# Kernel tuning notes

Hardware: AMD Instinct MI355X
Metric: run time of the kernel (lower is better)

Reference implementation:

```python
import jax, jax.numpy as jnp
import numpy as np

B = 128                      # num_graphs (cell lines per batch)
SIZES = [706, 512, 256, 128] # nodes per graph at each level; final_node = 128
DIM = 256                    # dim_cell
DEG = 8                      # avg degree of gene-gene network
EPS = 1e-5                   # BatchNorm eps


def _build_graph():
    """Build per-graph edges (incl. self-loops, as GATConv adds) and predefined
    cluster assignments per layer, coarsening edges exactly like PyG max_pool
    (remove self-loops + coalesce). Replicated across B graphs with offsets."""
    rng = np.random.default_rng(0)
    e = rng.integers(0, SIZES[0], size=(2, SIZES[0] * DEG))
    e = e[:, e[0] != e[1]]
    e = np.unique(e, axis=1)
    edges, clusters = [], []
    cur = e
    for i in range(3):
        n_cur, n_next = SIZES[i], SIZES[i + 1]
        sl = np.arange(n_cur)
        e_sl = np.concatenate([cur, np.stack([sl, sl])], axis=1)  # add self-loops
        off = np.arange(B) * n_cur
        eg = (e_sl[:, None, :] + off[None, :, None]).reshape(2, -1)
        edges.append(eg.astype(np.int32))
        cl = np.concatenate([np.arange(n_next), rng.integers(0, n_next, size=n_cur - n_next)])
        rng.shuffle(cl)  # surjective cluster assignment n_cur -> n_next
        clg = (cl[None, :] + (np.arange(B) * n_next)[:, None]).reshape(-1)
        clusters.append(clg.astype(np.int32))
        src, dst = cl[cur[0]], cl[cur[1]]
        m = src != dst                      # pool_edge: remove self-loops
        cur = np.unique(np.stack([src[m], dst[m]]), axis=1)  # coalesce
    return edges, clusters


def setup_inputs() -> dict:
    edges, clusters = _build_graph()
    key = jax.random.key(0)
    ks = jax.random.split(key, 16)
    d = {"x": jax.random.normal(ks[0], (B * SIZES[0], 3), jnp.float32)}
    ins = [3, DIM, DIM]
    for i in range(3):
        s = 1.0 / np.sqrt(ins[i])
        a = 1.0 / np.sqrt(DIM)
        d[f"W{i}"] = jax.random.normal(ks[1 + i], (ins[i], DIM), jnp.float32) * s
        d[f"asrc{i}"] = jax.random.normal(ks[4 + i], (DIM,), jnp.float32) * a
        d[f"adst{i}"] = jax.random.normal(ks[7 + i], (DIM,), jnp.float32) * a
        d[f"b{i}"] = jnp.zeros((DIM,), jnp.float32)
        d[f"edge{i}"] = jnp.asarray(edges[i])
        d[f"cluster{i}"] = jnp.asarray(clusters[i])
    return d


def _gat(x, edge, W, a_s, a_d, b):
    """PyG GATConv, heads=1, negative_slope=0.2 (self-loops pre-added in edge)."""
    N = x.shape[0]
    h = x @ W                                    # [N, D]
    src, dst = edge[0], edge[1]
    e = jax.nn.leaky_relu((h * a_s).sum(-1)[src] + (h * a_d).sum(-1)[dst], 0.2)
    m = jax.ops.segment_max(e, dst, num_segments=N)     # segment softmax (stable)
    ex = jnp.exp(e - m[dst])
    ssum = jax.ops.segment_sum(ex, dst, num_segments=N)
    alpha = ex / ssum[dst]
    out = jax.ops.segment_sum(h[src] * alpha[:, None], dst, num_segments=N)
    return out + b


def _forward(x, Ws, a_ss, a_ds, bs, edges, clusters):
    for i in range(3):
        x = jax.nn.relu(_gat(x, edges[i], Ws[i], a_ss[i], a_ds[i], bs[i]))
        # max_pool: scatter-max over predefined clusters (coarsen nodes)
        x = jax.ops.segment_max(x, clusters[i], num_segments=B * SIZES[i + 1])
        # BatchNorm1d(affine=False), training mode: biased batch stats
        mean = x.mean(0)
        var = x.var(0)
        x = (x - mean) * jax.lax.rsqrt(var + EPS)
    return x.reshape(B, SIZES[3] * DIM)


def reference(x, W0, W1, W2, asrc0, asrc1, asrc2, adst0, adst1, adst2,
              b0, b1, b2, edge0, edge1, edge2, cluster0, cluster1, cluster2):
    return _forward(x, (W0, W1, W2), (asrc0, asrc1, asrc2), (adst0, adst1, adst2),
                    (b0, b1, b2), (edge0, edge1, edge2), (cluster0, cluster1, cluster2))
```

## Files before the change

### kernel.cpp

```cpp
#include <hip/hip_runtime.h>
#include <hip/hip_fp16.h>

#define DIM 256
#define MAXMEM 16
#define MAXDEG 288

typedef _Float16 f16x8 __attribute__((ext_vector_type(8)));
typedef float f32x4 __attribute__((ext_vector_type(4)));

__device__ inline unsigned short f2h(float f) {
  return __half_as_ushort(__float2half_rn(f));
}
__device__ inline float h2f(unsigned short u) {
  return __half2float(__ushort_as_half(u));
}
__device__ inline __half2 hmax2_(__half2 a, __half2 b) {
  __half2 c;
  c.x = __hgt(a.x, b.x) ? a.x : b.x;
  c.y = __hgt(a.y, b.y) ? a.y : b.y;
  return c;
}


struct BktArgs {
  const int* esrc[3]; const int* edst[3]; const int* cl[3];
  int Eb[3]; int Nb[3]; int est[3];
  int* bdeg[3]; int* bccnt[3]; int* bebkt[3]; int* bcbkt[3];
};

__global__ __launch_bounds__(256) void l0_bucket(
    const float* __restrict__ x, const float* __restrict__ W,
    const float* __restrict__ asv, const float* __restrict__ adv,
    unsigned short* __restrict__ h, float* __restrict__ ssrc,
    float* __restrict__ sdst, int N, int Nb0, int l0Blocks, int bgx,
    BktArgs a) {
  if ((int)blockIdx.x >= l0Blocks) {
    int bb = blockIdx.x - l0Blocks;
    int L = bb / bgx;
    int i = (bb % bgx) * 256 + threadIdx.x;
    if (i < a.Eb[L]) {
      int d = a.edst[L][i];
      int slot = atomicAdd(&a.bdeg[L][d], 1);
      if (slot < a.est[L]) a.bebkt[L][d * a.est[L] + slot] = a.esrc[L][i];
    }
    if (i < a.Nb[L]) {
      int c = a.cl[L][i];
      int slot = atomicAdd(&a.bccnt[L][c], 1);
      if (slot < MAXMEM) a.bcbkt[L][c * MAXMEM + slot] = i;
    }
    return;
  }
  int wid = (blockIdx.x * 256 + threadIdx.x) >> 6;
  int lane = threadIdx.x & 63;
  if (wid >= N) return;
  int nb = wid >> 7, g = wid & 127;
  const float* xr = x + ((size_t)g * Nb0 + nb) * 3;
  float x0 = xr[0], x1 = xr[1], x2 = xr[2];
  int c = lane * 4;
  float4 w0 = *(const float4*)(W + c);
  float4 w1 = *(const float4*)(W + 256 + c);
  float4 w2 = *(const float4*)(W + 512 + c);
  float4 hv;
  hv.x = fmaf(x0, w0.x, fmaf(x1, w1.x, x2 * w2.x));
  hv.y = fmaf(x0, w0.y, fmaf(x1, w1.y, x2 * w2.y));
  hv.z = fmaf(x0, w0.z, fmaf(x1, w1.z, x2 * w2.z));
  hv.w = fmaf(x0, w0.w, fmaf(x1, w1.w, x2 * w2.w));
  ((ushort4*)(h + (size_t)wid * DIM))[lane] =
      make_ushort4(f2h(hv.x), f2h(hv.y), f2h(hv.z), f2h(hv.w));
  float4 a1 = ((const float4*)asv)[lane];
  float4 a2 = ((const float4*)adv)[lane];
  float d1 = hv.x * a1.x + hv.y * a1.y + hv.z * a1.z + hv.w * a1.w;
  float d2 = hv.x * a2.x + hv.y * a2.y + hv.z * a2.z + hv.w * a2.w;
  for (int o = 32; o > 0; o >>= 1) {
    d1 += __shfl_down(d1, o);
    d2 += __shfl_down(d2, o);
  }
  if (lane == 0) { ssrc[wid] = d1; sdst[wid] = d2; }
}

__global__ __launch_bounds__(256) void prep_k(
    const float* __restrict__ W, const float* __restrict__ sums,
    const float* __restrict__ sqs, float invN,
    unsigned short* __restrict__ Wt, float* __restrict__ cvec) {
  int n = blockIdx.x;
  int k = threadIdx.x;
  float mu = sums[k] * invN;
  float var = sqs[k] * invN - mu * mu;
  float istd = rsqrtf(var + 1e-5f);
  float w = W[(size_t)k * 256 + n] * istd;
  Wt[(size_t)n * 256 + k] = f2h(w);
  __shared__ float red[256];
  red[k] = mu * w;
  __syncthreads();
  for (int s = 128; s > 0; s >>= 1) {
    if (k < s) red[k] += red[k + s];
    __syncthreads();
  }
  if (k == 0) cvec[n] = -red[0];
}

__global__ __launch_bounds__(256) void gemm_mfma(
    const unsigned short* __restrict__ A, const unsigned short* __restrict__ Wt,
    const float* __restrict__ cvec, const float* __restrict__ asv,
    const float* __restrict__ adv, unsigned short* __restrict__ H,
    float* __restrict__ ssrc, float* __restrict__ sdst, int M) {
  __shared__ unsigned short Bs[2][256 * 32];
  int tid = threadIdx.x;
  int wave = tid >> 6, lane = tid & 63;
  int m0 = blockIdx.x * 128 + wave * 32;
  int row = lane & 15, quad = lane >> 4;

#pragma unroll
  for (int i = 0; i < 4; i++) {
    int c = i * 256 + tid;
    f16x8 v = *(const f16x8*)(const void*)(Wt + (size_t)(c >> 2) * 256 + (c & 3) * 8);
    *(f16x8*)(void*)(&Bs[0][c * 8]) = v;
  }
  __syncthreads();

  const unsigned short* Ap = A + (size_t)(m0 + row) * 256 + quad * 8;
  f32x4 acc[2][16] = {};
  for (int j = 0; j < 8; j++) {
    f16x8 pf[4];
    if (j < 7) {
#pragma unroll
      for (int i = 0; i < 4; i++) {
        int c = i * 256 + tid;
        pf[i] = *(const f16x8*)(const void*)(Wt + (size_t)(c >> 2) * 256 +
                                             (j + 1) * 32 + (c & 3) * 8);
      }
    }
    f16x8 a0 = *(const f16x8*)(const void*)(Ap + j * 32);
    f16x8 a1 = *(const f16x8*)(const void*)(Ap + 16 * 256 + j * 32);
    const unsigned short* bs = Bs[j & 1];
#pragma unroll
    for (int nt = 0; nt < 16; nt++) {
      f16x8 b = *(const f16x8*)(const void*)(bs + (nt * 16 + row) * 32 + quad * 8);
      acc[0][nt] = __builtin_amdgcn_mfma_f32_16x16x32_f16(a0, b, acc[0][nt], 0, 0, 0);
      acc[1][nt] = __builtin_amdgcn_mfma_f32_16x16x32_f16(a1, b, acc[1][nt], 0, 0, 0);
    }
    if (j < 7) {
#pragma unroll
      for (int i = 0; i < 4; i++) {
        int c = i * 256 + tid;
        *(f16x8*)(void*)(&Bs[(j + 1) & 1][c * 8]) = pf[i];
      }
    }
    __syncthreads();
  }

  float sav[16], sdv[16], cv[16];
#pragma unroll
  for (int nt = 0; nt < 16; nt++) {
    sav[nt] = asv[nt * 16 + row];
    sdv[nt] = adv[nt * 16 + row];
    cv[nt] = cvec[nt * 16 + row];
  }
#pragma unroll
  for (int sub = 0; sub < 2; sub++)
#pragma unroll
    for (int r = 0; r < 4; r++) {
      int mm = m0 + sub * 16 + quad * 4 + r;
      unsigned short* out = H + (size_t)mm * 256 + row;
      float d1 = 0.f, d2 = 0.f;
#pragma unroll
      for (int nt = 0; nt < 16; nt++) {
        float hv = acc[sub][nt][r] + cv[nt];
        out[nt * 16] = f2h(hv);
        d1 = fmaf(hv, sav[nt], d1);
        d2 = fmaf(hv, sdv[nt], d2);
      }
      for (int o = 1; o < 16; o <<= 1) {
        d1 += __shfl_xor(d1, o);
        d2 += __shfl_xor(d2, o);
      }
      if (row == 0) { ssrc[mm] = d1; sdst[mm] = d2; }
    }
}

__global__ __launch_bounds__(256) void gat_fused(
    const unsigned short* __restrict__ h, const int* __restrict__ bdeg,
    const int* __restrict__ bebkt, int estride,
    const int* __restrict__ bccnt, const int* __restrict__ bcbkt,
    const float* __restrict__ ssrc, const float* __restrict__ sdst,
    const float* __restrict__ bias, unsigned short* __restrict__ pooled,
    int Mb, int lgMb) {
  __shared__ float pLDS[MAXDEG * 8];
  __shared__ float psum[8];
  int b = blockIdx.x;
  int x = b & 7, t = b >> 3;
  int c = t & (Mb - 1);
  int set = x + 8 * (t >> lgMb);
  int tid = threadIdx.x;
  int gl = tid >> 5;
  int ch = tid & 31;
  int g = set * 8 + gl;
  int nm = bccnt[c]; if (nm > MAXMEM) nm = MAXMEM;
  float4 bf0 = *(const float4*)(bias + ch * 8);
  float4 bf1 = *(const float4*)(bias + ch * 8 + 4);
  __half2 hb[4] = {__floats2half2_rn(bf0.x, bf0.y), __floats2half2_rn(bf0.z, bf0.w),
                   __floats2half2_rn(bf1.x, bf1.y), __floats2half2_rn(bf1.z, bf1.w)};
  __half2 z = __float2half2_rn(0.f);
  __half2 best[4] = {z, z, z, z};
  for (int mi = 0; mi < nm; mi++) {
    int nb = __builtin_amdgcn_readfirstlane(bcbkt[c * MAXMEM + mi]);
    int deg = __builtin_amdgcn_readfirstlane(bdeg[nb]);
    if (deg > estride) deg = estride;
    const int* bk = bebkt + nb * estride;
    if (tid < 8) psum[tid] = 0.f;
    __syncthreads();
    for (int jj = tid; jj < deg * 8; jj += 256) {
      int j = jj >> 3, gi = jj & 7;
      int g2 = set * 8 + gi;
      int s = bk[j];
      float tt = ssrc[s * 128 + g2] + sdst[nb * 128 + g2];
      tt = tt > 0.f ? tt : 0.2f * tt;
      float p = __expf(tt);
      pLDS[jj] = p;
      atomicAdd(&psum[gi], p);
    }
    __syncthreads();
    float inv = 1.f / psum[gl];
    __half2 acc[4] = {z, z, z, z};
    int j = 0;
    for (; j + 4 <= deg; j += 4) {
      int4 ss = *(const int4*)(bk + j);
      __half2 hq0 = __float2half2_rn(pLDS[(j + 0) * 8 + gl] * inv);
      __half2 hq1 = __float2half2_rn(pLDS[(j + 1) * 8 + gl] * inv);
      __half2 hq2 = __float2half2_rn(pLDS[(j + 2) * 8 + gl] * inv);
      __half2 hq3 = __float2half2_rn(pLDS[(j + 3) * 8 + gl] * inv);
      uint4 v0 = *(const uint4*)(h + ((size_t)ss.x * 128 + g) * DIM + ch * 8);
      uint4 v1 = *(const uint4*)(h + ((size_t)ss.y * 128 + g) * DIM + ch * 8);
      uint4 v2 = *(const uint4*)(h + ((size_t)ss.z * 128 + g) * DIM + ch * 8);
      uint4 v3 = *(const uint4*)(h + ((size_t)ss.w * 128 + g) * DIM + ch * 8);
      union { uint4 u; __half2 p[4]; } u0, u1, u2, u3;
      u0.u = v0; u1.u = v1; u2.u = v2; u3.u = v3;
#pragma unroll
      for (int i = 0; i < 4; i++) {
        acc[i] = __hfma2(u0.p[i], hq0, acc[i]);
        acc[i] = __hfma2(u1.p[i], hq1, acc[i]);
        acc[i] = __hfma2(u2.p[i], hq2, acc[i]);
        acc[i] = __hfma2(u3.p[i], hq3, acc[i]);
      }
    }
    for (; j < deg; j++) {
      int s = bk[j];
      __half2 hq = __float2half2_rn(pLDS[j * 8 + gl] * inv);
      uint4 v0 = *(const uint4*)(h + ((size_t)s * 128 + g) * DIM + ch * 8);
      union { uint4 u; __half2 p[4]; } u0; u0.u = v0;
#pragma unroll
      for (int i = 0; i < 4; i++) acc[i] = __hfma2(u0.p[i], hq, acc[i]);
    }
#pragma unroll
    for (int i = 0; i < 4; i++)
      best[i] = hmax2_(best[i], __hadd2(acc[i], hb[i]));
    __syncthreads();
  }
  union { uint4 u; __half2 p[4]; } o;
#pragma unroll
  for (int i = 0; i < 4; i++) o.p[i] = best[i];
  *(uint4*)(pooled + ((size_t)c * 128 + g) * DIM + ch * 8) = o.u;
}

__global__ __launch_bounds__(256) void stats_k(
    const unsigned short* __restrict__ x, float* __restrict__ sums,
    float* __restrict__ sqs, int M) {
  int tid = threadIdx.x;
  int ch = tid & 31;
  int rg = tid >> 5;
  float s[8] = {}, q[8] = {};
  for (int r = blockIdx.x * 8 + rg; r < M; r += gridDim.x * 8) {
    uint4 v = *(const uint4*)(x + (size_t)r * DIM + ch * 8);
    union { uint4 u; __half2 p[4]; } uu; uu.u = v;
#pragma unroll
    for (int i = 0; i < 4; i++) {
      float2 f = __half22float2(uu.p[i]);
      s[2 * i]     += f.x; q[2 * i]     = fmaf(f.x, f.x, q[2 * i]);
      s[2 * i + 1] += f.y; q[2 * i + 1] = fmaf(f.y, f.y, q[2 * i + 1]);
    }
  }
  __shared__ float sm[512];
  sm[tid] = 0.f; sm[tid + 256] = 0.f;
  __syncthreads();
#pragma unroll
  for (int i = 0; i < 8; i++) {
    atomicAdd(&sm[ch * 8 + i], s[i]);
    atomicAdd(&sm[256 + ch * 8 + i], q[i]);
  }
  __syncthreads();
  atomicAdd(&sums[tid], sm[tid]);
  atomicAdd(&sqs[tid], sm[tid + 256]);
}

__global__ void norm_out(const unsigned short* __restrict__ xin,
                         float* __restrict__ xout,
                         const float* __restrict__ sums, const float* __restrict__ sqs,
                         float invN, int Mb, int total) {
  int idx = blockIdx.x * 256 + threadIdx.x;
  if (idx >= total) return;
  int ch = idx & 255;
  int r = idx >> 8;
  int g = r & 127, c = r >> 7;
  float mu = sums[ch] * invN;
  float var = sqs[ch] * invN - mu * mu;
  float v = (h2f(xin[idx]) - mu) * rsqrtf(var + 1e-5f);
  xout[((size_t)g * Mb + c) * 256 + ch] = v;
}

extern "C" void kernel_launch(void* const* d_in, const int* in_sizes, int n_in,
                              void* d_out, int out_size, void* d_ws, size_t ws_size,
                              hipStream_t stream) {
  const int B = 128;
  const int Nb[4] = {706, 512, 256, 128};
  const int Ns[4] = {128 * 706, 128 * 512, 128 * 256, 128 * 128};
  const int lgMb[3] = {9, 8, 7};
  const int EST[3] = {64, 160, 288};

  int iW[3], iA[3], iD[3], iB_[3], iE[3], iC[3];
  if (in_sizes[2] == 256) {
    for (int i = 0; i < 3; i++) {
      iW[i] = 1 + 6 * i; iA[i] = 2 + 6 * i; iD[i] = 3 + 6 * i;
      iB_[i] = 4 + 6 * i; iE[i] = 5 + 6 * i; iC[i] = 6 + 6 * i;
    }
  } else {
    for (int i = 0; i < 3; i++) {
      iW[i] = 1 + i; iA[i] = 4 + i; iD[i] = 7 + i;
      iB_[i] = 10 + i; iE[i] = 13 + i; iC[i] = 16 + i;
    }
  }
  int E[3];
  for (int i = 0; i < 3; i++) E[i] = in_sizes[iE[i]] / 2;

  int bebktOff[3], bcbktOff[3];
  size_t bebktTot = 0, bcbktTot = 0;
  for (int i = 0; i < 3; i++) {
    bebktOff[i] = (int)bebktTot; bebktTot += (size_t)Nb[i] * EST[i];
    bcbktOff[i] = (int)bcbktTot; bcbktTot += (size_t)Nb[i + 1] * MAXMEM;
  }

  char* wsp = (char*)d_ws;
  size_t o = 0;
  auto alloc = [&](size_t bytes) -> void* {
    void* p = wsp + o;
    o = (o + bytes + 255) & ~(size_t)255;
    return p;
  };
  unsigned short* h      = (unsigned short*)alloc((size_t)Ns[0] * DIM * 2);
  unsigned short* pooled = (unsigned short*)alloc((size_t)Ns[1] * DIM * 2);
  float* ssrc   = (float*)alloc((size_t)Ns[0] * 4);
  float* sdst   = (float*)alloc((size_t)Ns[0] * 4);
  float* statbuf= (float*)alloc(3 * 512 * 4);
  int*   bmeta  = (int*)alloc((size_t)3 * (Nb[0] + Nb[1]) * 4);
  char*  zend   = wsp + o;
  int*   bebkt  = (int*)alloc(bebktTot * 4);
  int*   bcbkt  = (int*)alloc(bcbktTot * 4);
  unsigned short* Wt = (unsigned short*)alloc(256 * 256 * 2);
  float* cvec   = (float*)alloc(256 * 4);
  (void)ws_size; (void)n_in; (void)out_size;

  const float* xin = (const float*)d_in[0];

  hipMemsetAsync(statbuf, 0, (size_t)(zend - (char*)statbuf), stream);

  BktArgs ba;
  int maxG = 0;
  for (int L = 0; L < 3; L++) {
    int Eb = E[L] / B;
    ba.esrc[L] = (const int*)d_in[iE[L]];
    ba.edst[L] = ba.esrc[L] + E[L];
    ba.cl[L]   = (const int*)d_in[iC[L]];
    ba.Eb[L] = Eb; ba.Nb[L] = Nb[L]; ba.est[L] = EST[L];
    ba.bdeg[L]  = bmeta + L * (Nb[0] + Nb[1]);
    ba.bccnt[L] = ba.bdeg[L] + Nb[L];
    ba.bebkt[L] = bebkt + bebktOff[L];
    ba.bcbkt[L] = bcbkt + bcbktOff[L];
    int gneed = (Eb > Nb[L] ? Eb : Nb[L]);
    if (gneed > maxG) maxG = gneed;
  }
  int bgx = (maxG + 255) / 256;

  for (int L = 0; L < 3; L++) {
    int N = Ns[L], M = Ns[L + 1];
    int NbL = Nb[L];
    const float* W  = (const float*)d_in[iW[L]];
    const float* av = (const float*)d_in[iA[L]];
    const float* dv = (const float*)d_in[iD[L]];
    const float* bv = (const float*)d_in[iB_[L]];
    float* sums = statbuf + L * 512;
    float* sqs  = sums + 256;
    int* bdeg = bmeta + L * (Nb[0] + Nb[1]);
    int* bccnt = bdeg + NbL;
    int* beb = bebkt + bebktOff[L];
    int* bcb = bcbkt + bcbktOff[L];

    if (L == 0) {
      int l0Blocks = (N + 3) / 4;
      l0_bucket<<<l0Blocks + bgx * 3, 256, 0, stream>>>(
          xin, W, av, dv, h, ssrc, sdst, N, NbL, l0Blocks, bgx, ba);
    } else {
      float* psums = statbuf + (L - 1) * 512;
      prep_k<<<256, 256, 0, stream>>>(W, psums, psums + 256, 1.0f / (float)N,
                                      Wt, cvec);
      gemm_mfma<<<N / 128, 256, 0, stream>>>(pooled, Wt, cvec, av, dv,
                                             h, ssrc, sdst, N);
    }

    int MbL = Nb[L + 1];
    gat_fused<<<MbL * 16, 256, 0, stream>>>(h, bdeg, beb, EST[L], bccnt, bcb,
                                            ssrc, sdst, bv, pooled,
                                            MbL, lgMb[L]);

    stats_k<<<512, 256, 0, stream>>>(pooled, sums, sqs, M);
  }

  norm_out<<<((size_t)Ns[3] * DIM + 255) / 256, 256, 0, stream>>>(
      pooled, (float*)d_out, statbuf + 2 * 512, statbuf + 2 * 512 + 256,
      1.0f / (float)Ns[3], Nb[3], Ns[3] * DIM);
}
```

Measured before the change: 344.1 us.

## Read GEMM weight tiles directly from global memory instead of LDS double-buffering

The GEMM kernel drops its shared-memory double buffer for the transposed weight matrix. Each wave now loads B fragments straight from global memory, relying on the L1/L2 caches, since every block reads the same 128 KB of weights. This removes the per-step syncthreads and the LDS staging stores. Launch bounds now request 2 blocks per CU. The trade is more global/cache traffic and the load latency sitting directly in the MFMA loop, in exchange for no LDS use, no barriers and possibly higher occupancy.

```diff
diff --git a/kernel.cpp b/kernel.cpp
--- a/kernel.cpp
+++ b/kernel.cpp
@@ -99,54 +99,29 @@
   if (k == 0) cvec[n] = -red[0];
 }
 
-__global__ __launch_bounds__(256) void gemm_mfma(
+__global__ __launch_bounds__(256, 2) void gemm_mfma(
     const unsigned short* __restrict__ A, const unsigned short* __restrict__ Wt,
     const float* __restrict__ cvec, const float* __restrict__ asv,
     const float* __restrict__ adv, unsigned short* __restrict__ H,
     float* __restrict__ ssrc, float* __restrict__ sdst, int M) {
-  __shared__ unsigned short Bs[2][256 * 32];
   int tid = threadIdx.x;
   int wave = tid >> 6, lane = tid & 63;
   int m0 = blockIdx.x * 128 + wave * 32;
   int row = lane & 15, quad = lane >> 4;
 
-#pragma unroll
-  for (int i = 0; i < 4; i++) {
-    int c = i * 256 + tid;
-    f16x8 v = *(const f16x8*)(const void*)(Wt + (size_t)(c >> 2) * 256 + (c & 3) * 8);
-    *(f16x8*)(void*)(&Bs[0][c * 8]) = v;
-  }
-  __syncthreads();
-
   const unsigned short* Ap = A + (size_t)(m0 + row) * 256 + quad * 8;
+  const unsigned short* Bp = Wt + (size_t)row * 256 + quad * 8;
   f32x4 acc[2][16] = {};
+#pragma unroll
   for (int j = 0; j < 8; j++) {
-    f16x8 pf[4];
-    if (j < 7) {
-#pragma unroll
-      for (int i = 0; i < 4; i++) {
-        int c = i * 256 + tid;
-        pf[i] = *(const f16x8*)(const void*)(Wt + (size_t)(c >> 2) * 256 +
-                                             (j + 1) * 32 + (c & 3) * 8);
-      }
-    }
     f16x8 a0 = *(const f16x8*)(const void*)(Ap + j * 32);
     f16x8 a1 = *(const f16x8*)(const void*)(Ap + 16 * 256 + j * 32);
-    const unsigned short* bs = Bs[j & 1];
 #pragma unroll
     for (int nt = 0; nt < 16; nt++) {
-      f16x8 b = *(const f16x8*)(const void*)(bs + (nt * 16 + row) * 32 + quad * 8);
+      f16x8 b = *(const f16x8*)(const void*)(Bp + (size_t)nt * 16 * 256 + j * 32);
       acc[0][nt] = __builtin_amdgcn_mfma_f32_16x16x32_f16(a0, b, acc[0][nt], 0, 0, 0);
       acc[1][nt] = __builtin_amdgcn_mfma_f32_16x16x32_f16(a1, b, acc[1][nt], 0, 0, 0);
     }
-    if (j < 7) {
-#pragma unroll
-      for (int i = 0; i < 4; i++) {
-        int c = i * 256 + tid;
-        *(f16x8*)(void*)(&Bs[(j + 1) & 1][c * 8]) = pf[i];
-      }
-    }
-    __syncthreads();
   }
 
   float sav[16], sdv[16], cv[16];
```

After: 375.3 us. 1.09x slower.
